# Performance work log

Measured on AMD Instinct MI355X. Metric: run time of the kernel, lower is better.

Reference implementation:

```python
import jax, jax.numpy as jnp
import numpy as np
from jax import lax

TAU = 2.0
VTH = 1.0
EPS = 1e-5


def heaviside(x):
    return (x >= 0.0).astype(x.dtype)


def lif_scan(x):
    """x: [T, ...]; LIF with decay_input=True, v_reset=0 (hard reset)."""
    def step(v, xt):
        v = v + (xt - v) / TAU
        s = heaviside(v - VTH)
        v = v * (1.0 - s)
        return v, s
    _, out = lax.scan(step, jnp.zeros_like(x[0]), x)
    return out


def conv2d(x, w):
    return lax.conv_general_dilated(x, w, (1, 1), 'SAME',
                                    dimension_numbers=('NCHW', 'OIHW', 'NCHW'))


def bn(x, g, b, m, v):
    inv = lax.rsqrt(v + EPS)
    return (x - m[None, :, None, None]) * (g * inv)[None, :, None, None] + b[None, :, None, None]


def maxpool2(x):
    return lax.reduce_window(x, -jnp.inf, lax.max, (1, 1, 2, 2), (1, 1, 2, 2), 'VALID')


def conv_block(x, w, g, b, m, v, pool):
    T, B = x.shape[:2]
    y = x.reshape((T * B,) + x.shape[2:])
    y = bn(conv2d(y, w), g, b, m, v)
    y = y.reshape((T, B) + y.shape[1:])
    y = lif_scan(y)
    if pool:
        y = y.reshape((T * B,) + y.shape[2:])
        y = maxpool2(y)
        y = y.reshape((T, B) + y.shape[1:])
    return y


def setup_inputs() -> dict:
    key = jax.random.key(0)
    ks = jax.random.split(key, 12)
    x = jax.random.normal(ks[0], (8, 128, 3, 32, 32), jnp.float32)
    w1 = jax.random.normal(ks[1], (64, 3, 3, 3), jnp.float32) * 0.1
    w2 = jax.random.normal(ks[2], (128, 64, 3, 3), jnp.float32) * 0.05
    w3 = jax.random.normal(ks[3], (256, 128, 3, 3), jnp.float32) * 0.05
    fc1_w = jax.random.normal(ks[4], (512, 16384), jnp.float32) * 0.01
    raw = jax.random.normal(ks[5], (10, 512), jnp.float32)
    Q, _ = jnp.linalg.qr(raw.T)  # 10 <= 512: orthogonal prototypes
    protos = Q.T[:10]
    d = dict(x=x, w1=w1, w2=w2, w3=w3, fc1_w=fc1_w, protos=protos)
    for i, c in zip((1, 2, 3), (64, 128, 256)):
        d[f'g{i}'] = jnp.ones((c,), jnp.float32)
        d[f'b{i}'] = jnp.zeros((c,), jnp.float32)
        d[f'm{i}'] = jax.random.normal(jax.random.fold_in(key, 100 + i), (c,), jnp.float32) * 0.1
        d[f'var{i}'] = jax.random.uniform(jax.random.fold_in(key, 200 + i), (c,), jnp.float32) + 0.5
    return d


def reference(x, w1, g1, b1, m1, var1, w2, g2, b2, m2, var2,
              w3, g3, b3, m3, var3, fc1_w, protos):
    h = conv_block(x, w1, g1, b1, m1, var1, pool=False)   # [T,B,64,32,32]
    h = conv_block(h, w2, g2, b2, m2, var2, pool=True)    # [T,B,128,16,16]
    h = conv_block(h, w3, g3, b3, m3, var3, pool=True)    # [T,B,256,8,8]
    T, B = h.shape[:2]
    h = h.reshape(T, B, -1)                               # [T,B,16384]
    h = jnp.einsum('tbd,fd->tbf', h, fc1_w)
    h = lif_scan(h)                                        # [T,B,512]
    feat = h.mean(axis=0)                                  # [B,512]
    fn = feat / jnp.clip(jnp.linalg.norm(feat, axis=1, keepdims=True), 1e-12)
    pn = protos / jnp.clip(jnp.linalg.norm(protos, axis=1, keepdims=True), 1e-12)
    return fn @ pn.T * 10.0                                # [B,10]
```

## Files before the change

### kernel.cpp

```cpp
#include <hip/hip_runtime.h>
#include <stdint.h>

#define EPS 1e-5f

typedef __attribute__((ext_vector_type(4))) float f32x4;
typedef __attribute__((ext_vector_type(8))) __bf16 bf16x8;

__device__ __forceinline__ void gl_lds16(const void* g, void* l) {
    __builtin_amdgcn_global_load_lds(
        (const __attribute__((address_space(1))) void*)g,
        (__attribute__((address_space(3))) void*)l, 16, 0, 0);
}

__device__ __forceinline__ unsigned short f2bf(float f) {
    unsigned u = __builtin_bit_cast(unsigned, f);
    unsigned r = (u + 0x7FFFu + ((u >> 16) & 1u)) >> 16;
    return (unsigned short)r;
}
__device__ __forceinline__ float bf2f(unsigned short h) {
    unsigned u = ((unsigned)h) << 16;
    return __builtin_bit_cast(float, u);
}

__device__ __forceinline__ uint4 expand8(unsigned int bt) {
    uint4 val;
    val.x = ((bt & 1u) ? 0x3F80u : 0u)  | ((bt & 2u) ? 0x3F800000u : 0u);
    val.y = ((bt & 4u) ? 0x3F80u : 0u)  | ((bt & 8u) ? 0x3F800000u : 0u);
    val.z = ((bt & 16u) ? 0x3F80u : 0u) | ((bt & 32u) ? 0x3F800000u : 0u);
    val.w = ((bt & 64u) ? 0x3F80u : 0u) | ((bt & 128u) ? 0x3F800000u : 0u);
    return val;
}

#define OFF_W2S   0ULL
#define OFF_W3S   442368ULL
#define OFF_FCS   2211840ULL
#define OFF_S1M   52543488ULL
#define OFF_S2PM  60932096ULL
#define OFF_S3    65126400ULL
#define OFF_PRE4P 98680832ULL
#define OFF_FEAT  115458048ULL
#define OFF_PN    115720192ULL

__global__ void repack_w2s(const float* __restrict__ w2, unsigned short* __restrict__ out) {
    int i = blockIdx.x * 256 + threadIdx.x;
    if (i >= 73728) return;
    int oc = i / 576, rem = i % 576;
    int ic = rem / 9, tap = rem % 9;
    float w = w2[i];
    unsigned short hi = f2bf(w);  float r1 = w - bf2f(hi);
    unsigned short md = f2bf(r1); float r2 = r1 - bf2f(md);
    unsigned short lo = f2bf(r2);
    size_t base = ((size_t)(tap * 128 + oc)) * 64 + (((ic >> 3) ^ (oc & 7)) << 3) + (ic & 7);
    out[base] = hi; out[base + 73728] = md; out[base + 147456] = lo;
}
__global__ void repack_w3s(const float* __restrict__ w3, unsigned short* __restrict__ out) {
    int i = blockIdx.x * 256 + threadIdx.x;
    if (i >= 294912) return;
    int oc = i / 1152, rem = i % 1152;
    int ic = rem / 9, tap = rem % 9;
    float w = w3[i];
    unsigned short hi = f2bf(w);  float r1 = w - bf2f(hi);
    unsigned short md = f2bf(r1); float r2 = r1 - bf2f(md);
    unsigned short lo = f2bf(r2);
    int cc = tap * 2 + (ic >> 6), icl = ic & 63;
    size_t base = ((size_t)(cc * 256 + oc)) * 64 + (((icl >> 3) ^ (oc & 7)) << 3) + (icl & 7);
    out[base] = hi; out[base + 294912] = md; out[base + 589824] = lo;
}
__global__ void repack_fcs(const float* __restrict__ fw, unsigned short* __restrict__ out) {
    int i = blockIdx.x * 256 + threadIdx.x;
    if (i >= 8388608) return;
    int f = i >> 14, d = i & 16383;
    float w = fw[i];
    unsigned short hi = f2bf(w);  float r1 = w - bf2f(hi);
    unsigned short md = f2bf(r1); float r2 = r1 - bf2f(md);
    unsigned short lo = f2bf(r2);
    int cc = d >> 6, kl = d & 63;
    size_t base = (((size_t)cc << 9) + f) * 64 + (((kl >> 3) ^ (f & 7)) << 3) + (kl & 7);
    out[base] = hi; out[base + 8388608] = md; out[base + 16777216] = lo;
}

__global__ __launch_bounds__(256) void conv1_lif_pack(
    const float* __restrict__ x, const float* __restrict__ w1,
    const float* __restrict__ g1, const float* __restrict__ b1,
    const float* __restrict__ m1, const float* __restrict__ var1,
    unsigned long long* __restrict__ s1m)
{
    __shared__ float xt[3][3][40];
    int blk = blockIdx.x;
    int b = blk >> 5, y = blk & 31;
    int tid = threadIdx.x;
    int w = tid >> 6, lane = tid & 63;

    float wr[27];
#pragma unroll
    for (int j = 0; j < 27; ++j) wr[j] = w1[lane * 27 + j];
    float scale = g1[lane] / sqrtf(var1[lane] + EPS);
    float bias  = b1[lane] - m1[lane] * scale;

    float v[8];
#pragma unroll
    for (int p = 0; p < 8; ++p) v[p] = 0.f;

    for (int t = 0; t < 8; ++t) {
        __syncthreads();
        const float* xb = x + ((size_t)(t * 128 + b)) * 3072;
        for (int i = tid; i < 360; i += 256) {
            int ic = i / 120, rem = i % 120, dr = rem / 40, col = rem % 40;
            int yy = y + dr - 1, xx = col - 4;
            float val = 0.f;
            if (yy >= 0 && yy < 32 && xx >= 0 && xx < 32)
                val = xb[ic * 1024 + yy * 32 + xx];
            xt[ic][dr][col] = val;
        }
        __syncthreads();

        float acc[8];
#pragma unroll
        for (int p = 0; p < 8; ++p) acc[p] = 0.f;
#pragma unroll
        for (int ic = 0; ic < 3; ++ic)
#pragma unroll
        for (int dr = 0; dr < 3; ++dr) {
            const float* row = &xt[ic][dr][w * 8];
            float bf[16];
            *(float4*)&bf[0]  = *(const float4*)&row[0];
            *(float4*)&bf[4]  = *(const float4*)&row[4];
            *(float4*)&bf[8]  = *(const float4*)&row[8];
            *(float4*)&bf[12] = *(const float4*)&row[12];
#pragma unroll
            for (int p = 0; p < 8; ++p)
#pragma unroll
                for (int dxm = 0; dxm < 3; ++dxm)
                    acc[p] += bf[p + dxm + 3] * wr[ic * 9 + dr * 3 + dxm];
        }
        size_t base = ((size_t)t * 128 + b) * 1024 + y * 32 + w * 8;
#pragma unroll
        for (int p = 0; p < 8; ++p) {
            float pre = acc[p] * scale + bias;
            v[p] = v[p] + (pre - v[p]) * 0.5f;
            bool s = (v[p] >= 1.0f);
            unsigned long long mk = __ballot(s);
            if (s) v[p] = 0.f;
            if (lane == 0) s1m[base + p] = mk;
        }
    }
}

__global__ __launch_bounds__(512, 2) void conv2_mfma(
    const unsigned long long* __restrict__ s1m,
    const unsigned short* __restrict__ w2s,
    const float* __restrict__ g, const float* __restrict__ bb,
    const float* __restrict__ mm, const float* __restrict__ vv,
    unsigned long long* __restrict__ s2pm)
{
    __shared__ unsigned long long mt[2][340];
    __shared__ unsigned short Aexp[340 * 64];
    __shared__ unsigned short Bt[2][3 * 8192];
    __shared__ unsigned short pm16[4][16][8];

    int tid = threadIdx.x;
    int m0 = blockIdx.x << 8;
    int b = m0 >> 10;
    int pix0 = m0 & 1023;
    int y0 = pix0 >> 5;

    int w = tid >> 6, lane = tid & 63;
    int wm = w & 3, wn = w >> 2;
    int q = lane >> 4, r = lane & 15;
    int swr = r & 7;

    int yloc[4], xloc[4];
#pragma unroll
    for (int i = 0; i < 4; ++i) {
        int mrow = wm * 64 + i * 16 + r;
        yloc[i] = mrow >> 5; xloc[i] = mrow & 31;
    }

    float scl[4], bia[4];
#pragma unroll
    for (int j = 0; j < 4; ++j) {
        int oc = wn * 64 + j * 16 + r;
        float s0 = g[oc] / sqrtf(vv[oc] + EPS);
        scl[j] = s0;
        bia[j] = bb[oc] - mm[oc] * s0;
    }

    float vr[4][4][4];
#pragma unroll
    for (int i = 0; i < 4; ++i)
#pragma unroll
        for (int j = 0; j < 4; ++j)
#pragma unroll
            for (int k = 0; k < 4; ++k) vr[i][j][k] = 0.f;

    const char* w2sb = (const char*)w2s;
    char* Btb = (char*)Bt;

    for (int i = tid; i < 340; i += 512) {
        int ly = i / 34, lx = i % 34;
        int yy = y0 + ly - 1, xx = lx - 1;
        unsigned long long mv = 0ULL;
        if (yy >= 0 && yy < 32 && xx >= 0 && xx < 32)
            mv = s1m[(b << 10) + (yy << 5) + xx];
        mt[0][i] = mv;
    }
#pragma unroll
    for (int s = 0; s < 3; ++s)
#pragma unroll
        for (int p = 0; p < 2; ++p)
            gl_lds16(w2sb + s * 147456 + p * 8192 + (w << 10) + (lane << 4),
                     Btb + s * 16384 + p * 8192 + (w << 10));
    __syncthreads();

    int pp = 0;
    for (int t = 0; t < 8; ++t) {
        {
            const unsigned long long* mtc = mt[t & 1];
            for (int u = tid; u < 680; u += 512) {
                int p = u >> 1, hc = u & 1;
                unsigned long long mk = mtc[p];
                unsigned int w32 = (unsigned int)(mk >> (hc << 5));
#pragma unroll
                for (int c4 = 0; c4 < 4; ++c4) {
                    int c = (hc << 2) + c4;
                    *(uint4*)((char*)Aexp + p * 128 + ((c ^ (p & 7)) << 4)) =
                        expand8(w32 >> (c4 << 3));
                }
            }
        }
        if (t < 7) {
            for (int i = tid; i < 340; i += 512) {
                int ly = i / 34, lx = i % 34;
                int yy = y0 + ly - 1, xx = lx - 1;
                unsigned long long mv = 0ULL;
                if (yy >= 0 && yy < 32 && xx >= 0 && xx < 32)
                    mv = s1m[(size_t)(t + 1) * 131072 + (b << 10) + (yy << 5) + xx];
                mt[(t + 1) & 1][i] = mv;
            }
        }
        __syncthreads();

        f32x4 acc[4][4];
#pragma unroll
        for (int i = 0; i < 4; ++i)
#pragma unroll
            for (int j = 0; j < 4; ++j) acc[i][j] = (f32x4){0.f, 0.f, 0.f, 0.f};

        for (int tap = 0; tap < 9; ++tap) {
            int dy = tap / 3, dx = tap - dy * 3;
            {
                int tap2 = (tap == 8) ? 0 : (tap + 1);
                const char* gb = w2sb + tap2 * 16384 + (w << 10) + (lane << 4);
                char* lb = Btb + (pp ^ 1) * 49152 + (w << 10);
#pragma unroll
                for (int s = 0; s < 3; ++s)
#pragma unroll
                    for (int p = 0; p < 2; ++p)
                        gl_lds16(gb + s * 147456 + p * 8192, lb + s * 16384 + p * 8192);
            }
            const char* Bc = Btb + pp * 49152;
#pragma unroll
            for (int ks = 0; ks < 2; ++ks) {
                bf16x8 af[4];
#pragma unroll
                for (int i = 0; i < 4; ++i) {
                    int p3 = (yloc[i] + dy) * 34 + xloc[i] + dx;
                    af[i] = *(const bf16x8*)((const char*)Aexp + p3 * 128 +
                             ((((ks << 2) + q) ^ (p3 & 7)) << 4));
                }
#pragma unroll
                for (int s = 0; s < 3; ++s) {
                    bf16x8 bfr[4];
#pragma unroll
                    for (int j = 0; j < 4; ++j)
                        bfr[j] = *(const bf16x8*)(Bc + s * 16384 + (wn * 64 + j * 16 + r) * 128 +
                                 ((((ks << 2) + q) ^ swr) << 4));
#pragma unroll
                    for (int i = 0; i < 4; ++i)
#pragma unroll
                        for (int j = 0; j < 4; ++j)
                            acc[i][j] = __builtin_amdgcn_mfma_f32_16x16x32_bf16(af[i], bfr[j], acc[i][j], 0, 0, 0);
                }
            }
            __syncthreads();
            pp ^= 1;
        }

        unsigned long long S = 0ULL;
#pragma unroll
        for (int i = 0; i < 4; ++i)
#pragma unroll
            for (int j = 0; j < 4; ++j)
#pragma unroll
                for (int reg = 0; reg < 4; ++reg) {
                    float pre = acc[i][j][reg] * scl[j] + bia[j];
                    float vo = vr[i][j][reg];
                    vo = vo + (pre - vo) * 0.5f;
                    bool sp = (vo >= 1.0f);
                    vr[i][j][reg] = sp ? 0.f : vo;
                    if (sp) S |= 1ULL << (i * 16 + j * 4 + reg);
                }
#pragma unroll
        for (int b1 = 0; b1 < 2; ++b1)
#pragma unroll
            for (int u = 0; u < 2; ++u)
#pragma unroll
                for (int j = 0; j < 4; ++j) {
                    int k0 = b1 * 16 + j * 4 + 2 * u;
                    bool sp = (((S >> k0) | (S >> (k0 + 1)) | (S >> (k0 + 32)) | (S >> (k0 + 33))) & 1ULL) != 0;
                    unsigned long long mk = __ballot(sp);
                    if (r == 0)
                        pm16[wm][b1 * 8 + (q << 1) + u][wn * 4 + j] = (unsigned short)(mk >> (q << 4));
                }
        __syncthreads();
        if (tid < 128) {
            int py = tid >> 5, px = (tid >> 1) & 15, h = tid & 1;
            unsigned long long vmk = *(unsigned long long*)&pm16[py][px][h << 2];
            s2pm[(size_t)t * 65536 + ((size_t)(b << 8) + ((y0 >> 1) + py) * 16 + px) * 2 + h] = vmk;
        }
    }
}

__global__ __launch_bounds__(512, 2) void conv3_mfma(
    const unsigned long long* __restrict__ s2pm,
    const unsigned short* __restrict__ w3s,
    const float* __restrict__ g, const float* __restrict__ bb,
    const float* __restrict__ mm, const float* __restrict__ vv,
    unsigned short* __restrict__ s3)
{
    __shared__ unsigned long long mt3[2][324][2];
    __shared__ unsigned short Aexp[324 * 64];
    __shared__ unsigned short Bt[2][3 * 8192];

    int tid = threadIdx.x;
    int b = blockIdx.x;
    int n0 = blockIdx.y << 7;

    int w = tid >> 6, lane = tid & 63;
    int wm = w & 3, wn = w >> 2;
    int q = lane >> 4, r = lane & 15;
    int swr = r & 7;

    float scl[4], bia[4];
#pragma unroll
    for (int j = 0; j < 4; ++j) {
        int oc = n0 + wn * 64 + j * 16 + r;
        float s0 = g[oc] / sqrtf(vv[oc] + EPS);
        scl[j] = s0;
        bia[j] = bb[oc] - mm[oc] * s0;
    }

    float vr[4][4][4];
#pragma unroll
    for (int i = 0; i < 4; ++i)
#pragma unroll
        for (int j = 0; j < 4; ++j)
#pragma unroll
            for (int k = 0; k < 4; ++k) vr[i][j][k] = 0.f;

    const char* w3sb = (const char*)w3s;
    char* Btb = (char*)Bt;
    int bsw = b & 7;

    for (int i = tid; i < 648; i += 512) {
        int p = i >> 1, hh = i & 1;
        int ly = p / 18, lx = p % 18;
        int yy = ly - 1, xx = lx - 1;
        unsigned long long mv = 0ULL;
        if (yy >= 0 && yy < 16 && xx >= 0 && xx < 16)
            mv = s2pm[((size_t)(b << 8) + (yy << 4) + xx) * 2 + hh];
        mt3[0][p][hh] = mv;
    }
#pragma unroll
    for (int s = 0; s < 3; ++s)
#pragma unroll
        for (int p = 0; p < 2; ++p)
            gl_lds16(w3sb + s * 589824 + n0 * 128 + p * 8192 + (w << 10) + (lane << 4),
                     Btb + s * 16384 + p * 8192 + (w << 10));
    __syncthreads();

    int pp = 0;
    for (int t = 0; t < 8; ++t) {
        {
            for (int u = tid; u < 648; u += 512) {
                int p = u >> 1, hc = u & 1;
                unsigned long long mk = mt3[t & 1][p][0];
                unsigned int w32 = (unsigned int)(mk >> (hc << 5));
#pragma unroll
                for (int c4 = 0; c4 < 4; ++c4) {
                    int c = (hc << 2) + c4;
                    *(uint4*)((char*)Aexp + p * 128 + ((c ^ (p & 7)) << 4)) =
                        expand8(w32 >> (c4 << 3));
                }
            }
        }
        if (t < 7) {
            for (int i = tid; i < 648; i += 512) {
                int p = i >> 1, hh = i & 1;
                int ly = p / 18, lx = p % 18;
                int yy = ly - 1, xx = lx - 1;
                unsigned long long mv = 0ULL;
                if (yy >= 0 && yy < 16 && xx >= 0 && xx < 16)
                    mv = s2pm[(size_t)(t + 1) * 65536 + ((size_t)(b << 8) + (yy << 4) + xx) * 2 + hh];
                mt3[(t + 1) & 1][p][hh] = mv;
            }
        }
        __syncthreads();

        f32x4 acc[4][4];
#pragma unroll
        for (int i = 0; i < 4; ++i)
#pragma unroll
            for (int j = 0; j < 4; ++j) acc[i][j] = (f32x4){0.f, 0.f, 0.f, 0.f};

        for (int h = 0; h < 2; ++h) {
            for (int tap = 0; tap < 9; ++tap) {
                int dy = tap / 3, dx = tap - dy * 3;
                int cc = tap * 2 + h;
                {
                    int ncc = (tap < 8) ? (cc + 2) : ((h == 0) ? 1 : 0);
                    const char* gb = w3sb + ncc * 32768 + n0 * 128 + (w << 10) + (lane << 4);
                    char* lb = Btb + (pp ^ 1) * 49152 + (w << 10);
#pragma unroll
                    for (int s = 0; s < 3; ++s)
#pragma unroll
                        for (int p = 0; p < 2; ++p)
                            gl_lds16(gb + s * 589824 + p * 8192, lb + s * 16384 + p * 8192);
                }
                const char* Bc = Btb + pp * 49152;
#pragma unroll
                for (int ks = 0; ks < 2; ++ks) {
                    bf16x8 af[4];
#pragma unroll
                    for (int i = 0; i < 4; ++i) {
                        int p3 = (wm * 4 + i + dy) * 18 + r + dx;
                        af[i] = *(const bf16x8*)((const char*)Aexp + p3 * 128 +
                                 ((((ks << 2) + q) ^ (p3 & 7)) << 4));
                    }
#pragma unroll
                    for (int s = 0; s < 3; ++s) {
                        bf16x8 bfr[4];
#pragma unroll
                        for (int j = 0; j < 4; ++j)
                            bfr[j] = *(const bf16x8*)(Bc + s * 16384 + (wn * 64 + j * 16 + r) * 128 +
                                     ((((ks << 2) + q) ^ swr) << 4));
#pragma unroll
                        for (int i = 0; i < 4; ++i)
#pragma unroll
                            for (int j = 0; j < 4; ++j)
                                acc[i][j] = __builtin_amdgcn_mfma_f32_16x16x32_bf16(af[i], bfr[j], acc[i][j], 0, 0, 0);
                    }
                }
                __syncthreads();
                pp ^= 1;
            }
            if (h == 0) {
                for (int u = tid; u < 648; u += 512) {
                    int p = u >> 1, hc = u & 1;
                    unsigned long long mk = mt3[t & 1][p][1];
                    unsigned int w32 = (unsigned int)(mk >> (hc << 5));
#pragma unroll
                    for (int c4 = 0; c4 < 4; ++c4) {
                        int c = (hc << 2) + c4;
                        *(uint4*)((char*)Aexp + p * 128 + ((c ^ (p & 7)) << 4)) =
                            expand8(w32 >> (c4 << 3));
                    }
                }
                __syncthreads();
            }
        }

        unsigned long long S = 0ULL;
#pragma unroll
        for (int i = 0; i < 4; ++i)
#pragma unroll
            for (int j = 0; j < 4; ++j)
#pragma unroll
                for (int reg = 0; reg < 4; ++reg) {
                    float pre = acc[i][j][reg] * scl[j] + bia[j];
                    float vo = vr[i][j][reg];
                    vo = vo + (pre - vo) * 0.5f;
                    bool sp = (vo >= 1.0f);
                    vr[i][j][reg] = sp ? 0.f : vo;
                    if (sp) S |= 1ULL << (i * 16 + j * 4 + reg);
                }
        unsigned short* s3t = s3 + (size_t)t * 2097152;
#pragma unroll
        for (int a2 = 0; a2 < 2; ++a2)
#pragma unroll
            for (int u = 0; u < 2; ++u)
#pragma unroll
                for (int j = 0; j < 4; ++j) {
                    int kA = 32 * a2 + j * 4 + 2 * u;
                    bool sp = (((S >> kA) | (S >> (kA + 1)) | (S >> (kA + 16)) | (S >> (kA + 17))) & 1ULL) != 0;
                    int oc = n0 + wn * 64 + j * 16 + r;
                    int y2 = wm * 2 + a2;
                    int x2 = (q << 1) + u;
                    s3t[(size_t)(b << 14) + oc * 64 + ((y2 ^ bsw) << 3) + x2] =
                        (unsigned short)(sp ? 0x3F80 : 0);
                }
    }
}

__global__ __launch_bounds__(256, 2) void fc_mfma(
    const unsigned short* __restrict__ s3,
    const unsigned short* __restrict__ fcs,
    float* __restrict__ pre4p)
{
    __shared__ unsigned short A[128 * 64];
    __shared__ unsigned short B[3 * 128 * 64];

    int tid = threadIdx.x;
    int m0 = blockIdx.x << 7;
    int n0 = blockIdx.y << 7;
    int kseg = blockIdx.z;
    int cc0 = kseg << 5;

    int w = tid >> 6, lane = tid & 63;
    int wm = w & 1, wn = w >> 1;
    int q = lane >> 4, r = lane & 15;
    int swr = r & 7;

    f32x4 acc[4][4];
#pragma unroll
    for (int i = 0; i < 4; ++i)
#pragma unroll
        for (int j = 0; j < 4; ++j) acc[i][j] = (f32x4){0.f, 0.f, 0.f, 0.f};

    const char* s3b = (const char*)s3;
    const char* fcsb = (const char*)fcs;

    for (int cc = cc0; cc < cc0 + 32; ++cc) {
        __syncthreads();
        {
            char* lb = (char*)A + (w << 12);
#pragma unroll
            for (int p = 0; p < 4; ++p)
                gl_lds16(s3b + (size_t)(m0 + w * 32 + p * 8 + (lane >> 3)) * 32768
                             + cc * 128 + ((lane & 7) << 4),
                         lb + (p << 10));
        }
        {
            const char* gb = fcsb + cc * 65536 + n0 * 128 + (w << 12) + (lane << 4);
            char* lb = (char*)B + (w << 12);
#pragma unroll
            for (int s = 0; s < 3; ++s)
#pragma unroll
                for (int p = 0; p < 4; ++p)
                    gl_lds16(gb + s * 16777216 + (p << 10), lb + s * 16384 + (p << 10));
        }
        __syncthreads();
#pragma unroll
        for (int ks = 0; ks < 2; ++ks) {
            bf16x8 af[4];
#pragma unroll
            for (int i = 0; i < 4; ++i)
                af[i] = *(const bf16x8*)((const char*)A + (wm * 64 + i * 16 + r) * 128 + ((((ks << 2) + q) ^ swr) << 4));
#pragma unroll
            for (int s = 0; s < 3; ++s) {
                bf16x8 bfr[4];
#pragma unroll
                for (int j = 0; j < 4; ++j)
                    bfr[j] = *(const bf16x8*)((const char*)B + s * 16384 + (wn * 64 + j * 16 + r) * 128 + ((((ks << 2) + q) ^ swr) << 4));
#pragma unroll
                for (int i = 0; i < 4; ++i)
#pragma unroll
                    for (int j = 0; j < 4; ++j)
                        acc[i][j] = __builtin_amdgcn_mfma_f32_16x16x32_bf16(af[i], bfr[j], acc[i][j], 0, 0, 0);
            }
        }
    }
#pragma unroll
    for (int i = 0; i < 4; ++i) {
#pragma unroll
        for (int j = 0; j < 4; ++j) {
            size_t base = ((size_t)kseg * 1024 + m0 + wm * 64 + i * 16 + (q << 2)) * 512
                        + n0 + wn * 64 + j * 16 + r;
#pragma unroll
            for (int reg = 0; reg < 4; ++reg)
                pre4p[base + (size_t)reg * 512] = acc[i][j][reg];
        }
    }
}

__global__ void lif4_mean(const float* __restrict__ P, float* __restrict__ feat) {
    int i = blockIdx.x * 256 + threadIdx.x;
    if (i >= 65536) return;
    int b = i >> 9, f = i & 511;
    float v = 0.f, sum = 0.f;
#pragma unroll
    for (int t = 0; t < 8; ++t) {
        float pre = 0.f;
#pragma unroll
        for (int s = 0; s < 8; ++s)
            pre += P[(size_t)s * 524288 + (size_t)(t * 128 + b) * 512 + f];
        v = v + (pre - v) * 0.5f;
        if (v >= 1.0f) { sum += 1.f; v = 0.f; }
    }
    feat[i] = sum * 0.125f;
}

__global__ void protos_norm(const float* __restrict__ P, float* __restrict__ pn) {
    int p = blockIdx.x;
    int lane = threadIdx.x;
    float ss = 0.f;
    for (int f = lane; f < 512; f += 64) { float x = P[p * 512 + f]; ss += x * x; }
#pragma unroll
    for (int o = 32; o > 0; o >>= 1) ss += __shfl_xor(ss, o);
    float inv = 1.f / fmaxf(sqrtf(ss), 1e-12f);
    for (int f = lane; f < 512; f += 64) pn[p * 512 + f] = P[p * 512 + f] * inv;
}

__global__ void final_logits(const float* __restrict__ feat, const float* __restrict__ pn,
                             float* __restrict__ out) {
    int b = blockIdx.x;
    int lane = threadIdx.x;
    float fr[8];
    float ss = 0.f;
#pragma unroll
    for (int j = 0; j < 8; ++j) { fr[j] = feat[b * 512 + j * 64 + lane]; ss += fr[j] * fr[j]; }
#pragma unroll
    for (int o = 32; o > 0; o >>= 1) ss += __shfl_xor(ss, o);
    float inv = 10.f / fmaxf(sqrtf(ss), 1e-12f);
    for (int p = 0; p < 10; ++p) {
        float d = 0.f;
#pragma unroll
        for (int j = 0; j < 8; ++j) d += fr[j] * pn[p * 512 + j * 64 + lane];
#pragma unroll
        for (int o = 32; o > 0; o >>= 1) d += __shfl_xor(d, o);
        if (lane == 0) out[b * 10 + p] = d * inv;
    }
}

extern "C" void kernel_launch(void* const* d_in, const int* in_sizes, int n_in,
                              void* d_out, int out_size, void* d_ws, size_t ws_size,
                              hipStream_t stream) {
    const float* x      = (const float*)d_in[0];
    const float* w1     = (const float*)d_in[1];
    const float* w2     = (const float*)d_in[2];
    const float* w3     = (const float*)d_in[3];
    const float* fc1    = (const float*)d_in[4];
    const float* protos = (const float*)d_in[5];
    const float* g1 = (const float*)d_in[6],  *b1 = (const float*)d_in[7];
    const float* m1 = (const float*)d_in[8],  *v1 = (const float*)d_in[9];
    const float* g2 = (const float*)d_in[10], *b2 = (const float*)d_in[11];
    const float* m2 = (const float*)d_in[12], *v2p = (const float*)d_in[13];
    const float* g3 = (const float*)d_in[14], *b3 = (const float*)d_in[15];
    const float* m3 = (const float*)d_in[16], *v3p = (const float*)d_in[17];

    char* ws = (char*)d_ws;
    unsigned short* w2s = (unsigned short*)(ws + OFF_W2S);
    unsigned short* w3s = (unsigned short*)(ws + OFF_W3S);
    unsigned short* fcs = (unsigned short*)(ws + OFF_FCS);
    unsigned long long* s1m  = (unsigned long long*)(ws + OFF_S1M);
    unsigned long long* s2pm = (unsigned long long*)(ws + OFF_S2PM);
    unsigned short* s3 = (unsigned short*)(ws + OFF_S3);
    float* pre4p = (float*)(ws + OFF_PRE4P);
    float* feat  = (float*)(ws + OFF_FEAT);
    float* pn    = (float*)(ws + OFF_PN);

    repack_w2s<<<288, 256, 0, stream>>>(w2, w2s);
    repack_w3s<<<1152, 256, 0, stream>>>(w3, w3s);
    repack_fcs<<<32768, 256, 0, stream>>>(fc1, fcs);

    conv1_lif_pack<<<4096, 256, 0, stream>>>(x, w1, g1, b1, m1, v1, s1m);
    conv2_mfma<<<512, 512, 0, stream>>>(s1m, w2s, g2, b2, m2, v2p, s2pm);
    conv3_mfma<<<dim3(128, 2), 512, 0, stream>>>(s2pm, w3s, g3, b3, m3, v3p, s3);

    fc_mfma<<<dim3(8, 4, 8), 256, 0, stream>>>(s3, fcs, pre4p);
    lif4_mean<<<256, 256, 0, stream>>>(pre4p, feat);
    protos_norm<<<10, 64, 0, stream>>>(protos, pn);
    final_logits<<<128, 64, 0, stream>>>(feat, pn, (float*)d_out);
}
```

Measured before the change: 938.2 us.

## Shrink conv2/conv3 tiles and double FC split-K for more parallel blocks

```diff
diff --git a/kernel.cpp b/kernel.cpp
--- a/kernel.cpp
+++ b/kernel.cpp
@@ -38,8 +38,8 @@
 #define OFF_S2PM  60932096ULL
 #define OFF_S3    65126400ULL
 #define OFF_PRE4P 98680832ULL
-#define OFF_FEAT  115458048ULL
-#define OFF_PN    115720192ULL
+#define OFF_FEAT  132235264ULL
+#define OFF_PN    132497408ULL
 
 __global__ void repack_w2s(const float* __restrict__ w2, unsigned short* __restrict__ out) {
     int i = blockIdx.x * 256 + threadIdx.x;
@@ -146,151 +146,145 @@
     }
 }
 
-__global__ __launch_bounds__(512, 2) void conv2_mfma(
+__global__ __launch_bounds__(256, 3) void conv2_mfma(
     const unsigned long long* __restrict__ s1m,
     const unsigned short* __restrict__ w2s,
     const float* __restrict__ g, const float* __restrict__ bb,
     const float* __restrict__ mm, const float* __restrict__ vv,
     unsigned long long* __restrict__ s2pm)
 {
-    __shared__ unsigned long long mt[2][340];
-    __shared__ unsigned short Aexp[340 * 64];
-    __shared__ unsigned short Bt[2][3 * 8192];
-    __shared__ unsigned short pm16[4][16][8];
+    __shared__ unsigned long long mt[136];
+    __shared__ unsigned short Aexp[136 * 64];
+    __shared__ unsigned short Bt[2][8192];
+    __shared__ unsigned short pm16[16][8];
 
     int tid = threadIdx.x;
-    int m0 = blockIdx.x << 8;
+    int m0 = blockIdx.x << 6;
     int b = m0 >> 10;
     int pix0 = m0 & 1023;
     int y0 = pix0 >> 5;
 
     int w = tid >> 6, lane = tid & 63;
-    int wm = w & 3, wn = w >> 2;
     int q = lane >> 4, r = lane & 15;
     int swr = r & 7;
 
     int yloc[4], xloc[4];
 #pragma unroll
     for (int i = 0; i < 4; ++i) {
-        int mrow = wm * 64 + i * 16 + r;
+        int mrow = i * 16 + r;
         yloc[i] = mrow >> 5; xloc[i] = mrow & 31;
     }
 
-    float scl[4], bia[4];
-#pragma unroll
-    for (int j = 0; j < 4; ++j) {
-        int oc = wn * 64 + j * 16 + r;
+    float scl[2], bia[2];
+#pragma unroll
+    for (int j = 0; j < 2; ++j) {
+        int oc = w * 32 + j * 16 + r;
         float s0 = g[oc] / sqrtf(vv[oc] + EPS);
         scl[j] = s0;
         bia[j] = bb[oc] - mm[oc] * s0;
     }
 
-    float vr[4][4][4];
+    float vr[4][2][4];
 #pragma unroll
     for (int i = 0; i < 4; ++i)
 #pragma unroll
-        for (int j = 0; j < 4; ++j)
+        for (int j = 0; j < 2; ++j)
 #pragma unroll
             for (int k = 0; k < 4; ++k) vr[i][j][k] = 0.f;
 
     const char* w2sb = (const char*)w2s;
     char* Btb = (char*)Bt;
 
-    for (int i = tid; i < 340; i += 512) {
+    for (int i = tid; i < 136; i += 256) {
         int ly = i / 34, lx = i % 34;
         int yy = y0 + ly - 1, xx = lx - 1;
         unsigned long long mv = 0ULL;
         if (yy >= 0 && yy < 32 && xx >= 0 && xx < 32)
             mv = s1m[(b << 10) + (yy << 5) + xx];
-        mt[0][i] = mv;
-    }
-#pragma unroll
-    for (int s = 0; s < 3; ++s)
-#pragma unroll
-        for (int p = 0; p < 2; ++p)
-            gl_lds16(w2sb + s * 147456 + p * 8192 + (w << 10) + (lane << 4),
-                     Btb + s * 16384 + p * 8192 + (w << 10));
+        mt[i] = mv;
+    }
+    {
+        const char* gb = w2sb + (w << 12) + (lane << 4);
+        char* lb = Btb + (w << 12);
+#pragma unroll
+        for (int p = 0; p < 4; ++p) gl_lds16(gb + (p << 10), lb + (p << 10));
+    }
     __syncthreads();
 
     int pp = 0;
     for (int t = 0; t < 8; ++t) {
-        {
-            const unsigned long long* mtc = mt[t & 1];
-            for (int u = tid; u < 680; u += 512) {
-                int p = u >> 1, hc = u & 1;
-                unsigned long long mk = mtc[p];
-                unsigned int w32 = (unsigned int)(mk >> (hc << 5));
-#pragma unroll
-                for (int c4 = 0; c4 < 4; ++c4) {
-                    int c = (hc << 2) + c4;
-                    *(uint4*)((char*)Aexp + p * 128 + ((c ^ (p & 7)) << 4)) =
-                        expand8(w32 >> (c4 << 3));
-                }
+        for (int u = tid; u < 272; u += 256) {
+            int p = u >> 1, hc = u & 1;
+            unsigned long long mk = mt[p];
+            unsigned int w32 = (unsigned int)(mk >> (hc << 5));
+#pragma unroll
+            for (int c4 = 0; c4 < 4; ++c4) {
+                int c = (hc << 2) + c4;
+                *(uint4*)((char*)Aexp + p * 128 + ((c ^ (p & 7)) << 4)) =
+                    expand8(w32 >> (c4 << 3));
             }
         }
+        __syncthreads();
         if (t < 7) {
-            for (int i = tid; i < 340; i += 512) {
+            for (int i = tid; i < 136; i += 256) {
                 int ly = i / 34, lx = i % 34;
                 int yy = y0 + ly - 1, xx = lx - 1;
                 unsigned long long mv = 0ULL;
                 if (yy >= 0 && yy < 32 && xx >= 0 && xx < 32)
                     mv = s1m[(size_t)(t + 1) * 131072 + (b << 10) + (yy << 5) + xx];
-                mt[(t + 1) & 1][i] = mv;
+                mt[i] = mv;
             }
         }
-        __syncthreads();
-
-        f32x4 acc[4][4];
+
+        f32x4 acc[4][2];
 #pragma unroll
         for (int i = 0; i < 4; ++i)
 #pragma unroll
-            for (int j = 0; j < 4; ++j) acc[i][j] = (f32x4){0.f, 0.f, 0.f, 0.f};
+            for (int j = 0; j < 2; ++j) acc[i][j] = (f32x4){0.f, 0.f, 0.f, 0.f};
 
         for (int tap = 0; tap < 9; ++tap) {
             int dy = tap / 3, dx = tap - dy * 3;
-            {
-                int tap2 = (tap == 8) ? 0 : (tap + 1);
-                const char* gb = w2sb + tap2 * 16384 + (w << 10) + (lane << 4);
-                char* lb = Btb + (pp ^ 1) * 49152 + (w << 10);
-#pragma unroll
-                for (int s = 0; s < 3; ++s)
-#pragma unroll
-                    for (int p = 0; p < 2; ++p)
-                        gl_lds16(gb + s * 147456 + p * 8192, lb + s * 16384 + p * 8192);
+#pragma unroll
+            for (int s = 0; s < 3; ++s) {
+                {
+                    int s2 = s + 1, tap2 = tap;
+                    if (s2 == 3) { s2 = 0; tap2 = tap + 1; if (tap2 == 9) tap2 = 0; }
+                    const char* gb = w2sb + s2 * 147456 + tap2 * 16384 + (w << 12) + (lane << 4);
+                    char* lb = Btb + ((pp ^ 1) << 14) + (w << 12);
+#pragma unroll
+                    for (int p = 0; p < 4; ++p) gl_lds16(gb + (p << 10), lb + (p << 10));
+                }
+                const char* Bc = Btb + (pp << 14);
+#pragma unroll
+                for (int ks = 0; ks < 2; ++ks) {
+                    bf16x8 af[4];
+#pragma unroll
+                    for (int i = 0; i < 4; ++i) {
+                        int p3 = (yloc[i] + dy) * 34 + xloc[i] + dx;
+                        af[i] = *(const bf16x8*)((const char*)Aexp + p3 * 128 +
+                                 ((((ks << 2) + q) ^ (p3 & 7)) << 4));
+                    }
+                    bf16x8 bfr[2];
+#pragma unroll
+                    for (int j = 0; j < 2; ++j)
+                        bfr[j] = *(const bf16x8*)(Bc + (w * 32 + j * 16 + r) * 128 +
+                                 ((((ks << 2) + q) ^ swr) << 4));
+#pragma unroll
+                    for (int i = 0; i < 4; ++i)
+#pragma unroll
+                        for (int j = 0; j < 2; ++j)
+                            acc[i][j] = __builtin_amdgcn_mfma_f32_16x16x32_bf16(af[i], bfr[j], acc[i][j], 0, 0, 0);
+                }
+                __syncthreads();
+                pp ^= 1;
             }
-            const char* Bc = Btb + pp * 49152;
-#pragma unroll
-            for (int ks = 0; ks < 2; ++ks) {
-                bf16x8 af[4];
-#pragma unroll
-                for (int i = 0; i < 4; ++i) {
-                    int p3 = (yloc[i] + dy) * 34 + xloc[i] + dx;
-                    af[i] = *(const bf16x8*)((const char*)Aexp + p3 * 128 +
-                             ((((ks << 2) + q) ^ (p3 & 7)) << 4));
-                }
-#pragma unroll
-                for (int s = 0; s < 3; ++s) {
-                    bf16x8 bfr[4];
-#pragma unroll
-                    for (int j = 0; j < 4; ++j)
-                        bfr[j] = *(const bf16x8*)(Bc + s * 16384 + (wn * 64 + j * 16 + r) * 128 +
-                                 ((((ks << 2) + q) ^ swr) << 4));
-#pragma unroll
-                    for (int i = 0; i < 4; ++i)
-#pragma unroll
-                        for (int j = 0; j < 4; ++j)
-                            acc[i][j] = __builtin_amdgcn_mfma_f32_16x16x32_bf16(af[i], bfr[j], acc[i][j], 0, 0, 0);
-                }
-            }
-            __syncthreads();
-            pp ^= 1;
-        }
-
-        unsigned long long S = 0ULL;
+        }
+
+        unsigned int S = 0;
 #pragma unroll
         for (int i = 0; i < 4; ++i)
 #pragma unroll
-            for (int j = 0; j < 4; ++j)
+            for (int j = 0; j < 2; ++j)
 #pragma unroll
                 for (int reg = 0; reg < 4; ++reg) {
                     float pre = acc[i][j][reg] * scl[j] + bia[j];
@@ -298,63 +292,64 @@
                     vo = vo + (pre - vo) * 0.5f;
                     bool sp = (vo >= 1.0f);
                     vr[i][j][reg] = sp ? 0.f : vo;
-                    if (sp) S |= 1ULL << (i * 16 + j * 4 + reg);
+                    if (sp) S |= 1u << (i * 8 + j * 4 + reg);
                 }
 #pragma unroll
         for (int b1 = 0; b1 < 2; ++b1)
 #pragma unroll
             for (int u = 0; u < 2; ++u)
 #pragma unroll
-                for (int j = 0; j < 4; ++j) {
-                    int k0 = b1 * 16 + j * 4 + 2 * u;
-                    bool sp = (((S >> k0) | (S >> (k0 + 1)) | (S >> (k0 + 32)) | (S >> (k0 + 33))) & 1ULL) != 0;
+                for (int j = 0; j < 2; ++j) {
+                    int k0 = b1 * 8 + j * 4 + 2 * u;
+                    bool sp = (((S >> k0) | (S >> (k0 + 1)) | (S >> (k0 + 16)) | (S >> (k0 + 17))) & 1u) != 0;
                     unsigned long long mk = __ballot(sp);
                     if (r == 0)
-                        pm16[wm][b1 * 8 + (q << 1) + u][wn * 4 + j] = (unsigned short)(mk >> (q << 4));
+                        pm16[b1 * 8 + (q << 1) + u][w * 2 + j] = (unsigned short)(mk >> (q << 4));
                 }
         __syncthreads();
-        if (tid < 128) {
-            int py = tid >> 5, px = (tid >> 1) & 15, h = tid & 1;
-            unsigned long long vmk = *(unsigned long long*)&pm16[py][px][h << 2];
-            s2pm[(size_t)t * 65536 + ((size_t)(b << 8) + ((y0 >> 1) + py) * 16 + px) * 2 + h] = vmk;
-        }
-    }
-}
-
-__global__ __launch_bounds__(512, 2) void conv3_mfma(
+        if (tid < 32) {
+            int px = tid >> 1, h = tid & 1;
+            unsigned long long vmk = *(unsigned long long*)&pm16[px][h << 2];
+            s2pm[(size_t)t * 65536 + ((size_t)(b << 8) + (y0 >> 1) * 16 + px) * 2 + h] = vmk;
+        }
+    }
+}
+
+__global__ __launch_bounds__(256, 3) void conv3_mfma(
     const unsigned long long* __restrict__ s2pm,
     const unsigned short* __restrict__ w3s,
     const float* __restrict__ g, const float* __restrict__ bb,
     const float* __restrict__ mm, const float* __restrict__ vv,
     unsigned short* __restrict__ s3)
 {
-    __shared__ unsigned long long mt3[2][324][2];
-    __shared__ unsigned short Aexp[324 * 64];
-    __shared__ unsigned short Bt[2][3 * 8192];
+    __shared__ unsigned long long mt3[108][2];
+    __shared__ unsigned short Aexp[108 * 64];
+    __shared__ unsigned short Bt[2][8192];
 
     int tid = threadIdx.x;
-    int b = blockIdx.x;
+    int bx = blockIdx.x;
+    int b = bx >> 2, seg = bx & 3;
+    int y0 = seg << 2;
     int n0 = blockIdx.y << 7;
 
     int w = tid >> 6, lane = tid & 63;
-    int wm = w & 3, wn = w >> 2;
     int q = lane >> 4, r = lane & 15;
     int swr = r & 7;
 
-    float scl[4], bia[4];
-#pragma unroll
-    for (int j = 0; j < 4; ++j) {
-        int oc = n0 + wn * 64 + j * 16 + r;
+    float scl[2], bia[2];
+#pragma unroll
+    for (int j = 0; j < 2; ++j) {
+        int oc = n0 + w * 32 + j * 16 + r;
         float s0 = g[oc] / sqrtf(vv[oc] + EPS);
         scl[j] = s0;
         bia[j] = bb[oc] - mm[oc] * s0;
     }
 
-    float vr[4][4][4];
+    float vr[4][2][4];
 #pragma unroll
     for (int i = 0; i < 4; ++i)
 #pragma unroll
-        for (int j = 0; j < 4; ++j)
+        for (int j = 0; j < 2; ++j)
 #pragma unroll
             for (int k = 0; k < 4; ++k) vr[i][j][k] = 0.f;
 
@@ -362,102 +357,90 @@
     char* Btb = (char*)Bt;
     int bsw = b & 7;
 
-    for (int i = tid; i < 648; i += 512) {
+    for (int i = tid; i < 216; i += 256) {
         int p = i >> 1, hh = i & 1;
         int ly = p / 18, lx = p % 18;
-        int yy = ly - 1, xx = lx - 1;
+        int yy = y0 + ly - 1, xx = lx - 1;
         unsigned long long mv = 0ULL;
         if (yy >= 0 && yy < 16 && xx >= 0 && xx < 16)
             mv = s2pm[((size_t)(b << 8) + (yy << 4) + xx) * 2 + hh];
-        mt3[0][p][hh] = mv;
-    }
-#pragma unroll
-    for (int s = 0; s < 3; ++s)
-#pragma unroll
-        for (int p = 0; p < 2; ++p)
-            gl_lds16(w3sb + s * 589824 + n0 * 128 + p * 8192 + (w << 10) + (lane << 4),
-                     Btb + s * 16384 + p * 8192 + (w << 10));
+        mt3[p][hh] = mv;
+    }
+    {
+        const char* gb = w3sb + n0 * 128 + (w << 12) + (lane << 4);
+        char* lb = Btb + (w << 12);
+#pragma unroll
+        for (int p = 0; p < 4; ++p) gl_lds16(gb + (p << 10), lb + (p << 10));
+    }
     __syncthreads();
 
     int pp = 0;
     for (int t = 0; t < 8; ++t) {
-        {
-            for (int u = tid; u < 648; u += 512) {
-                int p = u >> 1, hc = u & 1;
-                unsigned long long mk = mt3[t & 1][p][0];
-                unsigned int w32 = (unsigned int)(mk >> (hc << 5));
-#pragma unroll
-                for (int c4 = 0; c4 < 4; ++c4) {
-                    int c = (hc << 2) + c4;
-                    *(uint4*)((char*)Aexp + p * 128 + ((c ^ (p & 7)) << 4)) =
-                        expand8(w32 >> (c4 << 3));
-                }
+        for (int u = tid; u < 216; u += 256) {
+            int p = u >> 1, hc = u & 1;
+            unsigned long long mk = mt3[p][0];
+            unsigned int w32 = (unsigned int)(mk >> (hc << 5));
+#pragma unroll
+            for (int c4 = 0; c4 < 4; ++c4) {
+                int c = (hc << 2) + c4;
+                *(uint4*)((char*)Aexp + p * 128 + ((c ^ (p & 7)) << 4)) =
+                    expand8(w32 >> (c4 << 3));
             }
         }
-        if (t < 7) {
-            for (int i = tid; i < 648; i += 512) {
-                int p = i >> 1, hh = i & 1;
-                int ly = p / 18, lx = p % 18;
-                int yy = ly - 1, xx = lx - 1;
-                unsigned long long mv = 0ULL;
-                if (yy >= 0 && yy < 16 && xx >= 0 && xx < 16)
-                    mv = s2pm[(size_t)(t + 1) * 65536 + ((size_t)(b << 8) + (yy << 4) + xx) * 2 + hh];
-                mt3[(t + 1) & 1][p][hh] = mv;
-            }
-        }
         __syncthreads();
 
-        f32x4 acc[4][4];
+        f32x4 acc[4][2];
 #pragma unroll
         for (int i = 0; i < 4; ++i)
 #pragma unroll
-            for (int j = 0; j < 4; ++j) acc[i][j] = (f32x4){0.f, 0.f, 0.f, 0.f};
+            for (int j = 0; j < 2; ++j) acc[i][j] = (f32x4){0.f, 0.f, 0.f, 0.f};
 
         for (int h = 0; h < 2; ++h) {
             for (int tap = 0; tap < 9; ++tap) {
                 int dy = tap / 3, dx = tap - dy * 3;
                 int cc = tap * 2 + h;
-                {
-                    int ncc = (tap < 8) ? (cc + 2) : ((h == 0) ? 1 : 0);
-                    const char* gb = w3sb + ncc * 32768 + n0 * 128 + (w << 10) + (lane << 4);
-                    char* lb = Btb + (pp ^ 1) * 49152 + (w << 10);
-#pragma unroll
-                    for (int s = 0; s < 3; ++s)
-#pragma unroll
-                        for (int p = 0; p < 2; ++p)
-                            gl_lds16(gb + s * 589824 + p * 8192, lb + s * 16384 + p * 8192);
-                }
-                const char* Bc = Btb + pp * 49152;
-#pragma unroll
-                for (int ks = 0; ks < 2; ++ks) {
-                    bf16x8 af[4];
-#pragma unroll
-                    for (int i = 0; i < 4; ++i) {
-                        int p3 = (wm * 4 + i + dy) * 18 + r + dx;
-                        af[i] = *(const bf16x8*)((const char*)Aexp + p3 * 128 +
-                                 ((((ks << 2) + q) ^ (p3 & 7)) << 4));
+#pragma unroll
+                for (int s = 0; s < 3; ++s) {
+                    {
+                        int s2 = s + 1, cc2 = cc;
+                        if (s2 == 3) {
+                            s2 = 0; cc2 = cc + 2;
+                            if (cc2 >= 18) cc2 = (h == 0) ? 1 : 0;
+                        }
+                        const char* gb = w3sb + s2 * 589824 + cc2 * 32768 + n0 * 128 + (w << 12) + (lane << 4);
+                        char* lb = Btb + ((pp ^ 1) << 14) + (w << 12);
+#pragma unroll
+                        for (int p = 0; p < 4; ++p) gl_lds16(gb + (p << 10), lb + (p << 10));
                     }
-#pragma unroll
-                    for (int s = 0; s < 3; ++s) {
-                        bf16x8 bfr[4];
-#pragma unroll
-                        for (int j = 0; j < 4; ++j)
-                            bfr[j] = *(const bf16x8*)(Bc + s * 16384 + (wn * 64 + j * 16 + r) * 128 +
+                    const char* Bc = Btb + (pp << 14);
+#pragma unroll
+                    for (int ks = 0; ks < 2; ++ks) {
+                        bf16x8 af[4];
+#pragma unroll
+                        for (int i = 0; i < 4; ++i) {
+                            int p3 = (i + dy) * 18 + r + dx;
+                            af[i] = *(const bf16x8*)((const char*)Aexp + p3 * 128 +
+                                     ((((ks << 2) + q) ^ (p3 & 7)) << 4));
+                        }
+                        bf16x8 bfr[2];
+#pragma unroll
+                        for (int j = 0; j < 2; ++j)
+                            bfr[j] = *(const bf16x8*)(Bc + (w * 32 + j * 16 + r) * 128 +
                                      ((((ks << 2) + q) ^ swr) << 4));
 #pragma unroll
                         for (int i = 0; i < 4; ++i)
 #pragma unroll
-                            for (int j = 0; j < 4; ++j)
+                            for (int j = 0; j < 2; ++j)
                                 acc[i][j] = __builtin_amdgcn_mfma_f32_16x16x32_bf16(af[i], bfr[j], acc[i][j], 0, 0, 0);
                     }
-                }
-                __syncthreads();
-                pp ^= 1;
+                    __syncthreads();
+                    pp ^= 1;
+                }
             }
             if (h == 0) {
-                for (int u = tid; u < 648; u += 512) {
+                for (int u = tid; u < 216; u += 256) {
                     int p = u >> 1, hc = u & 1;
-                    unsigned long long mk = mt3[t & 1][p][1];
+                    unsigned long long mk = mt3[p][1];
                     unsigned int w32 = (unsigned int)(mk >> (hc << 5));
 #pragma unroll
                     for (int c4 = 0; c4 < 4; ++c4) {
@@ -467,14 +450,25 @@
                     }
                 }
                 __syncthreads();
+                if (t < 7) {
+                    for (int i = tid; i < 216; i += 256) {
+                        int p = i >> 1, hh = i & 1;
+                        int ly = p / 18, lx = p % 18;
+                        int yy = y0 + ly - 1, xx = lx - 1;
+                        unsigned long long mv = 0ULL;
+                        if (yy >= 0 && yy < 16 && xx >= 0 && xx < 16)
+                            mv = s2pm[(size_t)(t + 1) * 65536 + ((size_t)(b << 8) + (yy << 4) + xx) * 2 + hh];
+                        mt3[p][hh] = mv;
+                    }
+                }
             }
         }
 
-        unsigned long long S = 0ULL;
+        unsigned int S = 0;
 #pragma unroll
         for (int i = 0; i < 4; ++i)
 #pragma unroll
-            for (int j = 0; j < 4; ++j)
+            for (int j = 0; j < 2; ++j)
 #pragma unroll
                 for (int reg = 0; reg < 4; ++reg) {
                     float pre = acc[i][j][reg] * scl[j] + bia[j];
@@ -482,7 +476,7 @@
                     vo = vo + (pre - vo) * 0.5f;
                     bool sp = (vo >= 1.0f);
                     vr[i][j][reg] = sp ? 0.f : vo;
-                    if (sp) S |= 1ULL << (i * 16 + j * 4 + reg);
+                    if (sp) S |= 1u << (i * 8 + j * 4 + reg);
                 }
         unsigned short* s3t = s3 + (size_t)t * 2097152;
 #pragma unroll
@@ -490,11 +484,11 @@
 #pragma unroll
             for (int u = 0; u < 2; ++u)
 #pragma unroll
-                for (int j = 0; j < 4; ++j) {
-                    int kA = 32 * a2 + j * 4 + 2 * u;
-                    bool sp = (((S >> kA) | (S >> (kA + 1)) | (S >> (kA + 16)) | (S >> (kA + 17))) & 1ULL) != 0;
-                    int oc = n0 + wn * 64 + j * 16 + r;
-                    int y2 = wm * 2 + a2;
+                for (int j = 0; j < 2; ++j) {
+                    int kA = a2 * 16 + j * 4 + 2 * u;
+                    bool sp = (((S >> kA) | (S >> (kA + 1)) | (S >> (kA + 8)) | (S >> (kA + 9))) & 1u) != 0;
+                    int oc = n0 + w * 32 + j * 16 + r;
+                    int y2 = (y0 >> 1) + a2;
                     int x2 = (q << 1) + u;
                     s3t[(size_t)(b << 14) + oc * 64 + ((y2 ^ bsw) << 3) + x2] =
                         (unsigned short)(sp ? 0x3F80 : 0);
@@ -514,7 +508,7 @@
     int m0 = blockIdx.x << 7;
     int n0 = blockIdx.y << 7;
     int kseg = blockIdx.z;
-    int cc0 = kseg << 5;
+    int cc0 = kseg << 4;
 
     int w = tid >> 6, lane = tid & 63;
     int wm = w & 1, wn = w >> 1;
@@ -530,7 +524,7 @@
     const char* s3b = (const char*)s3;
     const char* fcsb = (const char*)fcs;
 
-    for (int cc = cc0; cc < cc0 + 32; ++cc) {
+    for (int cc = cc0; cc < cc0 + 16; ++cc) {
         __syncthreads();
         {
             char* lb = (char*)A + (w << 12);
@@ -592,7 +586,7 @@
     for (int t = 0; t < 8; ++t) {
         float pre = 0.f;
 #pragma unroll
-        for (int s = 0; s < 8; ++s)
+        for (int s = 0; s < 16; ++s)
             pre += P[(size_t)s * 524288 + (size_t)(t * 128 + b) * 512 + f];
         v = v + (pre - v) * 0.5f;
         if (v >= 1.0f) { sum += 1.f; v = 0.f; }
@@ -664,10 +658,10 @@
     repack_fcs<<<32768, 256, 0, stream>>>(fc1, fcs);
 
     conv1_lif_pack<<<4096, 256, 0, stream>>>(x, w1, g1, b1, m1, v1, s1m);
-    conv2_mfma<<<512, 512, 0, stream>>>(s1m, w2s, g2, b2, m2, v2p, s2pm);
-    conv3_mfma<<<dim3(128, 2), 512, 0, stream>>>(s2pm, w3s, g3, b3, m3, v3p, s3);
-
-    fc_mfma<<<dim3(8, 4, 8), 256, 0, stream>>>(s3, fcs, pre4p);
+    conv2_mfma<<<2048, 256, 0, stream>>>(s1m, w2s, g2, b2, m2, v2p, s2pm);
+    conv3_mfma<<<dim3(512, 2), 256, 0, stream>>>(s2pm, w3s, g3, b3, m3, v3p, s3);
+
+    fc_mfma<<<dim3(8, 4, 16), 256, 0, stream>>>(s3, fcs, pre4p);
     lif4_mean<<<256, 256, 0, stream>>>(pre4p, feat);
     protos_norm<<<10, 64, 0, stream>>>(protos, pn);
     final_logits<<<128, 64, 0, stream>>>(feat, pn, (float*)d_out);
```

After: 1.186 ms. 1.26x slower.
